# Kernel optimization log

Hardware: AMD Instinct MI355X
Metric: run time of the kernel (lower is better)

Reference implementation:

```python
import jax, jax.numpy as jnp
import numpy as np

N_USER, N_ITEM = 100000, 50000
E, L = 640000, 200000
F0, F1, F2 = 128, 128, 64


def _mean_agg(x_src, src, dst, n_dst):
    # gather messages from source nodes, mean-aggregate onto destination nodes
    msg = x_src[src]                                            # [E, F]
    s = jax.ops.segment_sum(msg, dst, num_segments=n_dst)       # [n_dst, F]
    cnt = jax.ops.segment_sum(jnp.ones((src.shape[0], 1), x_src.dtype), dst,
                              num_segments=n_dst)               # [n_dst, 1]
    return s / jnp.maximum(cnt, 1.0)


def _sage(x_src, x_dst, src, dst, n_dst, Wl, b, Wr):
    # PyG SAGEConv: lin_l(mean_aggr(x_src)) + lin_r(x_dst)
    agg = _mean_agg(x_src, src, dst, n_dst)
    return agg @ Wl + b + x_dst @ Wr


def setup_inputs() -> dict:
    key = jax.random.key(0)
    ks = jax.random.split(key, 20)
    inp = {}
    inp['x_user'] = jax.random.normal(ks[0], (N_USER, F0), jnp.float32)
    inp['x_item'] = jax.random.normal(ks[1], (N_ITEM, F0), jnp.float32)
    inp['src_u'] = jax.random.randint(ks[2], (E,), 0, N_USER)
    inp['dst_i'] = jax.random.randint(ks[3], (E,), 0, N_ITEM)
    inp['el_src'] = jax.random.randint(ks[4], (L,), 0, N_USER)
    inp['el_dst'] = jax.random.randint(ks[5], (L,), 0, N_ITEM)
    # SAGEConv params per edge type per layer: Wl (neighbor), bias, Wr (root)
    def w(k, fi, fo):
        return jax.random.normal(k, (fi, fo), jnp.float32) * (1.0 / np.sqrt(fi))
    inp['Wl_ui1'] = w(ks[6], F0, F1);  inp['b_ui1'] = jnp.zeros((F1,), jnp.float32)
    inp['Wr_ui1'] = w(ks[7], F0, F1)
    inp['Wl_iu1'] = w(ks[8], F0, F1);  inp['b_iu1'] = jnp.zeros((F1,), jnp.float32)
    inp['Wr_iu1'] = w(ks[9], F0, F1)
    inp['Wl_ui2'] = w(ks[10], F1, F2); inp['b_ui2'] = jnp.zeros((F2,), jnp.float32)
    inp['Wr_ui2'] = w(ks[11], F1, F2)
    inp['Wl_iu2'] = w(ks[12], F1, F2); inp['b_iu2'] = jnp.zeros((F2,), jnp.float32)
    inp['Wr_iu2'] = w(ks[13], F1, F2)
    return inp


def reference(x_user, x_item, src_u, dst_i, el_src, el_dst,
              Wl_ui1, b_ui1, Wr_ui1, Wl_iu1, b_iu1, Wr_iu1,
              Wl_ui2, b_ui2, Wr_ui2, Wl_iu2, b_iu2, Wr_iu2):
    # layer 1 (to_hetero: one SAGEConv per edge type; relu per node type; eval -> no dropout)
    h_i1 = jax.nn.relu(_sage(x_user, x_item, src_u, dst_i, N_ITEM, Wl_ui1, b_ui1, Wr_ui1))
    h_u1 = jax.nn.relu(_sage(x_item, x_user, dst_i, src_u, N_USER, Wl_iu1, b_iu1, Wr_iu1))
    # layer 2
    h_i2 = _sage(h_u1, h_i1, src_u, dst_i, N_ITEM, Wl_ui2, b_ui2, Wr_ui2)
    h_u2 = _sage(h_i1, h_u1, dst_i, src_u, N_USER, Wl_iu2, b_iu2, Wr_iu2)
    # LPsimple_classif: gather endpoints, elementwise product, sum over features
    pred = (h_u2[el_src] * h_i2[el_dst]).sum(axis=-1)           # [L]
    return pred
```

## Files before the change

### kernel.cpp

```cpp
#include <hip/hip_runtime.h>

#define NUSER 100000
#define NITEM 50000
#define NEDGE 640000
#define NLINK 200000
#define GI 49
#define GU 98
#define NBU 391
#define NBI 196
#define NBG1 (4 * (NBU + NBI))
#define NBG2 (2 * (NBU + NBI))
#define FCHUNK 4096
#define FNCH 157

typedef unsigned int  uint;
typedef unsigned short ushort_t;
typedef __attribute__((ext_vector_type(8))) short bf16x8;
typedef __attribute__((ext_vector_type(4))) float f32x4;
typedef __attribute__((ext_vector_type(4))) uint  u32x4;

__device__ __forceinline__ ushort_t f2bf(float f) {
    uint u = __float_as_uint(f);
    u += 0x7FFFu + ((u >> 16) & 1u);
    return (ushort_t)(u >> 16);
}
__device__ __forceinline__ float bf2f(ushort_t h) { return __uint_as_float(((uint)h) << 16); }
__device__ __forceinline__ float lo16f(uint u) { return __uint_as_float(u << 16); }
__device__ __forceinline__ float hi16f(uint u) { return __uint_as_float(u & 0xFFFF0000u); }

__global__ __launch_bounds__(256) void countw_kernel(
    const int* __restrict__ src, const int* __restrict__ dst,
    int* __restrict__ cnt_u, int* __restrict__ cnt_i,
    const float* __restrict__ Wl0, const float* __restrict__ Wr0,
    const float* __restrict__ Wl1, const float* __restrict__ Wr1,
    const float* __restrict__ Wl2, const float* __restrict__ Wr2,
    const float* __restrict__ Wl3, const float* __restrict__ Wr3,
    ushort_t* __restrict__ Bh0, ushort_t* __restrict__ Bl0,
    ushort_t* __restrict__ Bh1, ushort_t* __restrict__ Bl1,
    ushort_t* __restrict__ Bh2, ushort_t* __restrict__ Bl2,
    ushort_t* __restrict__ Bh3, ushort_t* __restrict__ Bl3)
{
    if (blockIdx.x < 2500) {
        int e = blockIdx.x * 256 + threadIdx.x;
        if (e >= NEDGE) return;
        atomicAdd(&cnt_u[src[e]], 1);
        atomicAdd(&cnt_i[dst[e]], 1);
        return;
    }
    int b = blockIdx.x - 2500;
    const float *Wl, *Wr; ushort_t *Bh, *Bl; int FO, t;
    if (b < 16)      { Wl = Wl0; Wr = Wr0; Bh = Bh0; Bl = Bl0; FO = 128; t = b * 256 + threadIdx.x; }
    else if (b < 32) { Wl = Wl1; Wr = Wr1; Bh = Bh1; Bl = Bl1; FO = 128; t = (b - 16) * 256 + threadIdx.x; }
    else if (b < 40) { Wl = Wl2; Wr = Wr2; Bh = Bh2; Bl = Bl2; FO = 64;  t = (b - 32) * 256 + threadIdx.x; }
    else             { Wl = Wl3; Wr = Wr3; Bh = Bh3; Bl = Bl3; FO = 64;  t = (b - 40) * 256 + threadIdx.x; }
    int lane = t & 63, ks = (t >> 6) & 3, nt = t >> 8;
    int col = nt * 16 + (lane & 15);
    int k0 = ks * 32 + (lane >> 4) * 8;
    const float* W = (col < FO) ? Wl : Wr;
    int cc = (col < FO) ? col : col - FO;
#pragma unroll
    for (int j = 0; j < 8; ++j) {
        float v = W[(size_t)(k0 + j) * FO + cc];
        ushort_t h = f2bf(v);
        Bh[(size_t)t * 8 + j] = h;
        Bl[(size_t)t * 8 + j] = f2bf(v - bf2f(h));
    }
}

__global__ __launch_bounds__(256) void scan1_kernel(
    const int* __restrict__ cnt_i, const int* __restrict__ cnt_u,
    int* __restrict__ head_i, int* __restrict__ head_u,
    int* __restrict__ bsum_i, int* __restrict__ bsum_u)
{
    __shared__ int sh[256];
    int b = blockIdx.x, t = threadIdx.x;
    const int* cnt; int* head; int* bsum; int n, cb;
    if (b < GI) { cnt = cnt_i; head = head_i; bsum = bsum_i; n = NITEM; cb = b; }
    else        { cnt = cnt_u; head = head_u; bsum = bsum_u; n = NUSER; cb = b - GI; }
    int base = cb * 1024 + t * 4;
    int4 v = {0, 0, 0, 0};
    if (base + 3 < n) v = *(const int4*)(cnt + base);
    else {
        if (base + 0 < n) v.x = cnt[base + 0];
        if (base + 1 < n) v.y = cnt[base + 1];
        if (base + 2 < n) v.z = cnt[base + 2];
    }
    int s = v.x + v.y + v.z + v.w;
    sh[t] = s;
    __syncthreads();
    for (int o = 1; o < 256; o <<= 1) {
        int a = (t >= o) ? sh[t - o] : 0;
        __syncthreads();
        sh[t] += a;
        __syncthreads();
    }
    int excl = sh[t] - s;
    if (t == 255) bsum[cb] = sh[255];
    if (base + 0 < n) head[base + 0] = excl;
    if (base + 1 < n) head[base + 1] = excl + v.x;
    if (base + 2 < n) head[base + 2] = excl + v.x + v.y;
    if (base + 3 < n) head[base + 3] = excl + v.x + v.y + v.z;
}

__global__ __launch_bounds__(256) void scan23_kernel(
    int* __restrict__ head_i, int* __restrict__ head_u,
    const int* __restrict__ bsum_i, const int* __restrict__ bsum_u)
{
    __shared__ int sh[256];
    int b = blockIdx.x, t = threadIdx.x;
    int* head; const int* bsum; int n, cb;
    if (b < GI) { head = head_i; bsum = bsum_i; n = NITEM; cb = b; }
    else        { head = head_u; bsum = bsum_u; n = NUSER; cb = b - GI; }
    sh[t] = (t < cb) ? bsum[t] : 0;
    __syncthreads();
    for (int o = 128; o >= 1; o >>= 1) {
        if (t < o) sh[t] += sh[t + o];
        __syncthreads();
    }
    int add = sh[0];
    int base = cb * 1024 + t * 4;
#pragma unroll
    for (int k = 0; k < 4; ++k)
        if (base + k < n) head[base + k] += add;
}

template <int OSTRIDE, bool ASPLIT>
__device__ __forceinline__ void gemm_body(
    const void* __restrict__ A_,
    const ushort_t* __restrict__ Bh, const ushort_t* __restrict__ Bl,
    ushort_t* __restrict__ dstp, int n, int row0,
    u32x4* __restrict__ bshH, u32x4* __restrict__ bshL)
{
    constexpr int NB = 1024;
    const u32x4* gh = (const u32x4*)Bh;
    const u32x4* gl = (const u32x4*)Bl;
#pragma unroll
    for (int i = 0; i < 2; ++i) {
        int idx = i * 512 + threadIdx.x;
        bshH[idx] = gh[idx];
        bshL[idx] = gl[idx];
    }
    __syncthreads();

    const int lane = threadIdx.x & 63, wv = threadIdx.x >> 6;
    const int lr = lane & 15, lg = lane >> 4;
    const int wrow0 = row0 + wv * 32;
    const int r0 = wrow0 + lr, r1 = wrow0 + 16 + lr;

    f32x4 acc[2][4];
#pragma unroll
    for (int rt = 0; rt < 2; ++rt)
#pragma unroll
        for (int ct = 0; ct < 4; ++ct) { f32x4 zz = {0.f, 0.f, 0.f, 0.f}; acc[rt][ct] = zz; }

    f32x4 f0c[2], f1c[2]; u32x4 qc[2];
#define LOAD_A(KS)                                                              \
    {                                                                           \
        int kb = (KS) * 32 + lg * 8;                                            \
        int rows[2] = {r0, r1};                                                 \
        _Pragma("unroll")                                                       \
        for (int rt = 0; rt < 2; ++rt) {                                        \
            if (ASPLIT) {                                                       \
                f0c[rt] = f32x4{0.f, 0.f, 0.f, 0.f};                            \
                f1c[rt] = f32x4{0.f, 0.f, 0.f, 0.f};                            \
                if (rows[rt] < n) {                                             \
                    const f32x4* p = (const f32x4*)((const float*)A_ +          \
                        (size_t)rows[rt] * 128 + kb);                           \
                    f0c[rt] = p[0]; f1c[rt] = p[1];                             \
                }                                                               \
            } else {                                                            \
                qc[rt] = u32x4{0u, 0u, 0u, 0u};                                 \
                if (rows[rt] < n)                                               \
                    qc[rt] = *(const u32x4*)((const ushort_t*)A_ +              \
                        (size_t)rows[rt] * 128 + kb);                           \
            }                                                                   \
        }                                                                       \
    }

    LOAD_A(0);
#pragma unroll
    for (int ks = 0; ks < 4; ++ks) {
        bf16x8 ah[2], al[2];
#pragma unroll
        for (int rt = 0; rt < 2; ++rt) {
            if (ASPLIT) {
                float e[8];
#pragma unroll
                for (int j = 0; j < 4; ++j) { e[j] = f0c[rt][j]; e[4 + j] = f1c[rt][j]; }
                uint hv[4], lv[4];
#pragma unroll
                for (int j = 0; j < 4; ++j) {
                    ushort_t h0 = f2bf(e[2 * j]), h1 = f2bf(e[2 * j + 1]);
                    hv[j] = (uint)h0 | ((uint)h1 << 16);
                    ushort_t l0 = f2bf(e[2 * j] - bf2f(h0)), l1 = f2bf(e[2 * j + 1] - bf2f(h1));
                    lv[j] = (uint)l0 | ((uint)l1 << 16);
                }
                u32x4 hq = {hv[0], hv[1], hv[2], hv[3]};
                u32x4 lq = {lv[0], lv[1], lv[2], lv[3]};
                ah[rt] = __builtin_bit_cast(bf16x8, hq);
                al[rt] = __builtin_bit_cast(bf16x8, lq);
            } else {
                ah[rt] = __builtin_bit_cast(bf16x8, qc[rt]);
            }
        }
        if (ks < 3) LOAD_A(ks + 1);

#pragma unroll
        for (int ct = 0; ct < 4; ++ct) {
            bf16x8 bh = __builtin_bit_cast(bf16x8, bshH[(ct * 4 + ks) * 64 + lane]);
            bf16x8 bl = __builtin_bit_cast(bf16x8, bshL[(ct * 4 + ks) * 64 + lane]);
#pragma unroll
            for (int rt = 0; rt < 2; ++rt) {
                acc[rt][ct] = __builtin_amdgcn_mfma_f32_16x16x32_bf16(ah[rt], bh, acc[rt][ct], 0, 0, 0);
                acc[rt][ct] = __builtin_amdgcn_mfma_f32_16x16x32_bf16(ah[rt], bl, acc[rt][ct], 0, 0, 0);
                if (ASPLIT)
                    acc[rt][ct] = __builtin_amdgcn_mfma_f32_16x16x32_bf16(al[rt], bh, acc[rt][ct], 0, 0, 0);
            }
        }
    }
#undef LOAD_A

#pragma unroll
    for (int rt = 0; rt < 2; ++rt)
#pragma unroll
        for (int ct = 0; ct < 4; ++ct) {
            int cc = ct * 16 + lr;
#pragma unroll
            for (int r = 0; r < 4; ++r) {
                int orow = wrow0 + rt * 16 + lg * 4 + r;
                if (orow < n) dstp[(size_t)orow * OSTRIDE + cc] = f2bf(acc[rt][ct][r]);
            }
        }
}

__global__ __launch_bounds__(512) void gemmfill_kernel(
    const float* __restrict__ xu, const float* __restrict__ xi,
    const ushort_t* __restrict__ Bh0, const ushort_t* __restrict__ Bl0,
    const ushort_t* __restrict__ Bh1, const ushort_t* __restrict__ Bl1,
    ushort_t* __restrict__ y0, ushort_t* __restrict__ z0,
    ushort_t* __restrict__ y1, ushort_t* __restrict__ z1,
    const int* __restrict__ src, const int* __restrict__ dst,
    int* __restrict__ head_i, int* __restrict__ head_u,
    int* __restrict__ nbr_i, int* __restrict__ nbr_u)
{
    if (blockIdx.x >= NBG1) {
        int b = blockIdx.x - NBG1;
        int pass = b / (2 * FNCH);
        int rem  = b % (2 * FNCH);
        int dir  = rem / FNCH;
        int base = (rem % FNCH) * FCHUNK;
        int e_end = min(base + FCHUNK, NEDGE);
        if (dir == 0) {
            int lo = pass * (NITEM / 8), hi = lo + NITEM / 8;
            for (int e = base + threadIdx.x; e < e_end; e += 512) {
                int d = dst[e];
                if (d >= lo && d < hi) nbr_i[atomicAdd(&head_i[d], 1)] = src[e];
            }
        } else {
            int lo = pass * (NUSER / 8), hi = lo + NUSER / 8;
            for (int e = base + threadIdx.x; e < e_end; e += 512) {
                int s = src[e];
                if (s >= lo && s < hi) nbr_u[atomicAdd(&head_u[s], 1)] = dst[e];
            }
        }
        return;
    }
    __shared__ u32x4 bshH[1024];
    __shared__ u32x4 bshL[1024];
    int bid = blockIdx.x;
    const float* A; const ushort_t *Bh, *Bl; ushort_t *yb, *zb; int n, rowblk, cg;
    if (bid < 4 * NBU) { A = xu; Bh = Bh0; Bl = Bl0; yb = y0; zb = z0; n = NUSER; rowblk = bid >> 2; cg = bid & 3; }
    else { int b2 = bid - 4 * NBU; A = xi; Bh = Bh1; Bl = Bl1; yb = y1; zb = z1; n = NITEM; rowblk = b2 >> 2; cg = b2 & 3; }
    ushort_t* dstp = ((cg < 2) ? yb : zb) + (cg & 1) * 64;
    gemm_body<128, true>(A, Bh + (size_t)cg * 8192, Bl + (size_t)cg * 8192,
                         dstp, n, rowblk * 256, bshH, bshL);
}

__global__ __launch_bounds__(512) void gemm2_kernel(
    const ushort_t* __restrict__ A0, const ushort_t* __restrict__ A1,
    const ushort_t* __restrict__ Bh0, const ushort_t* __restrict__ Bl0,
    const ushort_t* __restrict__ Bh1, const ushort_t* __restrict__ Bl1,
    ushort_t* __restrict__ y0, ushort_t* __restrict__ z0,
    ushort_t* __restrict__ y1, ushort_t* __restrict__ z1)
{
    __shared__ u32x4 bshH[1024];
    __shared__ u32x4 bshL[1024];
    int bid = blockIdx.x;
    const ushort_t* A; const ushort_t *Bh, *Bl; ushort_t *yb, *zb; int n, rowblk, cg;
    if (bid < 2 * NBU) { A = A0; Bh = Bh0; Bl = Bl0; yb = y0; zb = z0; n = NUSER; rowblk = bid >> 1; cg = bid & 1; }
    else { int b2 = bid - 2 * NBU; A = A1; Bh = Bh1; Bl = Bl1; yb = y1; zb = z1; n = NITEM; rowblk = b2 >> 1; cg = b2 & 1; }
    ushort_t* dstp = cg ? zb : yb;
    gemm_body<64, false>(A, Bh + (size_t)cg * 8192, Bl + (size_t)cg * 8192,
                         dstp, n, rowblk * 256, bshH, bshL);
}

__global__ __launch_bounds__(256) void gather1_kernel(
    const ushort_t* __restrict__ ymsg_u, const ushort_t* __restrict__ ymsg_i,
    const int* __restrict__ nbr_i, const int* __restrict__ head_i, const int* __restrict__ cnt_i,
    const int* __restrict__ nbr_u, const int* __restrict__ head_u, const int* __restrict__ cnt_u,
    const ushort_t* __restrict__ z_i, const ushort_t* __restrict__ z_u,
    const float* __restrict__ b_ui, const float* __restrict__ b_iu,
    ushort_t* __restrict__ h1_i, ushort_t* __restrict__ h1_u)
{
    int w = (blockIdx.x << 2) + (threadIdx.x >> 6);
    const ushort_t *ym, *z; const int *nbr, *head, *cnt; const float* bias;
    ushort_t* hout; int node;
    if (w < NITEM) { ym = ymsg_u; nbr = nbr_i; head = head_i; cnt = cnt_i; z = z_i; bias = b_ui; hout = h1_i; node = w; }
    else if (w < NITEM + NUSER) { ym = ymsg_i; nbr = nbr_u; head = head_u; cnt = cnt_u; z = z_u; bias = b_iu; hout = h1_u; node = w - NITEM; }
    else return;
    int lane = threadIdx.x & 63;
    int c = cnt[node], end = head[node];
    int j = end - c;
    const uint* Y = (const uint*)ym;
    float ax = 0.f, ay = 0.f;
    for (; j + 7 < end; j += 8) {
        uint u0 = Y[(size_t)nbr[j + 0] * 64 + lane];
        uint u1 = Y[(size_t)nbr[j + 1] * 64 + lane];
        uint u2 = Y[(size_t)nbr[j + 2] * 64 + lane];
        uint u3 = Y[(size_t)nbr[j + 3] * 64 + lane];
        uint u4 = Y[(size_t)nbr[j + 4] * 64 + lane];
        uint u5 = Y[(size_t)nbr[j + 5] * 64 + lane];
        uint u6 = Y[(size_t)nbr[j + 6] * 64 + lane];
        uint u7 = Y[(size_t)nbr[j + 7] * 64 + lane];
        ax += lo16f(u0) + lo16f(u1) + lo16f(u2) + lo16f(u3)
            + lo16f(u4) + lo16f(u5) + lo16f(u6) + lo16f(u7);
        ay += hi16f(u0) + hi16f(u1) + hi16f(u2) + hi16f(u3)
            + hi16f(u4) + hi16f(u5) + hi16f(u6) + hi16f(u7);
    }
    for (; j + 1 < end; j += 2) {
        uint u0 = Y[(size_t)nbr[j + 0] * 64 + lane];
        uint u1 = Y[(size_t)nbr[j + 1] * 64 + lane];
        ax += lo16f(u0) + lo16f(u1);
        ay += hi16f(u0) + hi16f(u1);
    }
    if (j < end) {
        uint u0 = Y[(size_t)nbr[j] * 64 + lane];
        ax += lo16f(u0); ay += hi16f(u0);
    }
    float m = 1.f / fmaxf((float)c, 1.f);
    uint zu = ((const uint*)z)[(size_t)node * 64 + lane];
    float vx = fmaxf(ax * m + lo16f(zu) + bias[lane * 2], 0.f);
    float vy = fmaxf(ay * m + hi16f(zu) + bias[lane * 2 + 1], 0.f);
    ((uint*)hout)[(size_t)node * 64 + lane] = (uint)f2bf(vx) | ((uint)f2bf(vy) << 16);
}

__global__ __launch_bounds__(256) void gather2_kernel(
    const ushort_t* __restrict__ ymsg_u, const ushort_t* __restrict__ ymsg_i,
    const int* __restrict__ nbr_i, const int* __restrict__ head_i, const int* __restrict__ cnt_i,
    const int* __restrict__ nbr_u, const int* __restrict__ head_u, const int* __restrict__ cnt_u,
    const ushort_t* __restrict__ z_i, const ushort_t* __restrict__ z_u,
    const float* __restrict__ b_ui, const float* __restrict__ b_iu,
    ushort_t* __restrict__ h2_i, ushort_t* __restrict__ h2_u)
{
    int w = (blockIdx.x << 2) + (threadIdx.x >> 6);
    const ushort_t *ym, *z; const int *nbr, *head, *cnt; const float* bias;
    ushort_t* hout; int node;
    if (w < NITEM) { ym = ymsg_u; nbr = nbr_i; head = head_i; cnt = cnt_i; z = z_i; bias = b_ui; hout = h2_i; node = w; }
    else if (w < NITEM + NUSER) { ym = ymsg_i; nbr = nbr_u; head = head_u; cnt = cnt_u; z = z_u; bias = b_iu; hout = h2_u; node = w - NITEM; }
    else return;
    int lane = threadIdx.x & 63;
    int c = cnt[node], end = head[node];
    int j = end - c;
    float a = 0.f;
    for (; j + 7 < end; j += 8) {
        a += bf2f(ym[(size_t)nbr[j + 0] * 64 + lane]) + bf2f(ym[(size_t)nbr[j + 1] * 64 + lane])
           + bf2f(ym[(size_t)nbr[j + 2] * 64 + lane]) + bf2f(ym[(size_t)nbr[j + 3] * 64 + lane])
           + bf2f(ym[(size_t)nbr[j + 4] * 64 + lane]) + bf2f(ym[(size_t)nbr[j + 5] * 64 + lane])
           + bf2f(ym[(size_t)nbr[j + 6] * 64 + lane]) + bf2f(ym[(size_t)nbr[j + 7] * 64 + lane]);
    }
    for (; j + 1 < end; j += 2)
        a += bf2f(ym[(size_t)nbr[j] * 64 + lane]) + bf2f(ym[(size_t)nbr[j + 1] * 64 + lane]);
    if (j < end) a += bf2f(ym[(size_t)nbr[j] * 64 + lane]);
    float m = 1.f / fmaxf((float)c, 1.f);
    float v = a * m + bf2f(z[(size_t)node * 64 + lane]) + bias[lane];
    hout[(size_t)node * 64 + lane] = f2bf(v);
}

__global__ __launch_bounds__(256) void predict_kernel(
    const int* __restrict__ el_src, const int* __restrict__ el_dst,
    const ushort_t* __restrict__ hu, const ushort_t* __restrict__ hi,
    float* __restrict__ out)
{
    int l = (blockIdx.x << 2) + (threadIdx.x >> 6);
    if (l >= NLINK) return;
    int lane = threadIdx.x & 63;
    int u = el_src[l];
    int it = el_dst[l];
    float v = bf2f(hu[(size_t)u * 64 + lane]) * bf2f(hi[(size_t)it * 64 + lane]);
#pragma unroll
    for (int o = 32; o >= 1; o >>= 1) v += __shfl_down(v, o, 64);
    if (lane == 0) out[l] = v;
}

extern "C" void kernel_launch(void* const* d_in, const int* in_sizes, int n_in,
                              void* d_out, int out_size, void* d_ws, size_t ws_size,
                              hipStream_t stream) {
    const float* x_user = (const float*)d_in[0];
    const float* x_item = (const float*)d_in[1];
    const int*   src_u  = (const int*)d_in[2];
    const int*   dst_i  = (const int*)d_in[3];
    const int*   el_src = (const int*)d_in[4];
    const int*   el_dst = (const int*)d_in[5];
    const float* Wl_ui1 = (const float*)d_in[6];
    const float* b_ui1  = (const float*)d_in[7];
    const float* Wr_ui1 = (const float*)d_in[8];
    const float* Wl_iu1 = (const float*)d_in[9];
    const float* b_iu1  = (const float*)d_in[10];
    const float* Wr_iu1 = (const float*)d_in[11];
    const float* Wl_ui2 = (const float*)d_in[12];
    const float* b_ui2  = (const float*)d_in[13];
    const float* Wr_ui2 = (const float*)d_in[14];
    const float* Wl_iu2 = (const float*)d_in[15];
    const float* b_iu2  = (const float*)d_in[16];
    const float* Wr_iu2 = (const float*)d_in[17];
    float* out = (float*)d_out;

    int* iw     = (int*)d_ws;
    int* cnt_i  = iw;
    int* cnt_u  = iw + 50000;
    int* bsum_i = iw + 150000;
    int* bsum_u = iw + 150064;
    int* head_i = iw + 150192;
    int* head_u = iw + 200192;
    int* nbr_i  = iw + 300192;
    int* nbr_u  = iw + 940192;
    char* W8 = (char*)d_ws;
    size_t off = 6320768;
    ushort_t* Bh1u = (ushort_t*)(W8 + off); off += 65536;
    ushort_t* Bl1u = (ushort_t*)(W8 + off); off += 65536;
    ushort_t* Bh1i = (ushort_t*)(W8 + off); off += 65536;
    ushort_t* Bl1i = (ushort_t*)(W8 + off); off += 65536;
    ushort_t* Bh2u = (ushort_t*)(W8 + off); off += 32768;
    ushort_t* Bl2u = (ushort_t*)(W8 + off); off += 32768;
    ushort_t* Bh2i = (ushort_t*)(W8 + off); off += 32768;
    ushort_t* Bl2i = (ushort_t*)(W8 + off); off += 32768;
    ushort_t* h1_u = (ushort_t*)(W8 + off); off += (size_t)NUSER * 128 * 2;
    ushort_t* h1_i = (ushort_t*)(W8 + off); off += (size_t)NITEM * 128 * 2;
    size_t YB = off;
    ushort_t* ymsg_u = (ushort_t*)(W8 + YB);
    ushort_t* ymsg_i = (ushort_t*)(W8 + YB + 25600000);
    ushort_t* z_u    = (ushort_t*)(W8 + YB + 38400000);
    ushort_t* z_i    = (ushort_t*)(W8 + YB + 64000000);
    ushort_t* ymsg2_u = (ushort_t*)(W8 + YB);
    ushort_t* ymsg2_i = (ushort_t*)(W8 + YB + 12800000);
    ushort_t* z2_u    = (ushort_t*)(W8 + YB + 19200000);
    ushort_t* z2_i    = (ushort_t*)(W8 + YB + 32000000);
    ushort_t* h2_u    = (ushort_t*)(W8 + YB + 38400000);
    ushort_t* h2_i    = (ushort_t*)(W8 + YB + 51200000);

    hipMemsetAsync(d_ws, 0, 150000 * sizeof(int), stream);

    countw_kernel<<<2548, 256, 0, stream>>>(
        src_u, dst_i, cnt_u, cnt_i,
        Wl_ui1, Wr_iu1, Wl_iu1, Wr_ui1, Wl_ui2, Wr_iu2, Wl_iu2, Wr_ui2,
        Bh1u, Bl1u, Bh1i, Bl1i, Bh2u, Bl2u, Bh2i, Bl2i);

    scan1_kernel<<<GI + GU, 256, 0, stream>>>(cnt_i, cnt_u, head_i, head_u, bsum_i, bsum_u);
    scan23_kernel<<<GI + GU, 256, 0, stream>>>(head_i, head_u, bsum_i, bsum_u);

    gemmfill_kernel<<<NBG1 + 8 * 2 * FNCH, 512, 0, stream>>>(
        x_user, x_item, Bh1u, Bl1u, Bh1i, Bl1i,
        ymsg_u, z_u, ymsg_i, z_i,
        src_u, dst_i, head_i, head_u, nbr_i, nbr_u);

    gather1_kernel<<<(NITEM + NUSER) / 4, 256, 0, stream>>>(
        ymsg_u, ymsg_i, nbr_i, head_i, cnt_i, nbr_u, head_u, cnt_u,
        z_i, z_u, b_ui1, b_iu1, h1_i, h1_u);

    gemm2_kernel<<<NBG2, 512, 0, stream>>>(
        h1_u, h1_i, Bh2u, Bl2u, Bh2i, Bl2i,
        ymsg2_u, z2_u, ymsg2_i, z2_i);
    gather2_kernel<<<(NITEM + NUSER) / 4, 256, 0, stream>>>(
        ymsg2_u, ymsg2_i, nbr_i, head_i, cnt_i, nbr_u, head_u, cnt_u,
        z2_i, z2_u, b_ui2, b_iu2, h2_i, h2_u);

    predict_kernel<<<NLINK / 4, 256, 0, stream>>>(el_src, el_dst, h2_u, h2_i, out);
}
```

Baseline: 370.9 us.

## Restructure layer-1 GEMM: truncation split, drop B-low term, LDS-staged stores, fewer fill passes

The layer-1 GEMM drops the A_hi*B_lo MFMA term and keeps only A_hi*B and A_lo*B, with A split by bit truncation instead of rounding. Each block now covers 128 rows by 128 columns with 8 column tiles per wave, and output is staged through LDS so global stores are coalesced 16-byte rows. The CSR fill uses 4 destination-range passes instead of 8. This cuts MFMA count, conversion ALU work, scattered 2-byte stores and redundant edge rereads, at the cost of some precision from omitting the weight low part and more atomic contention per pass.

```diff
diff --git a/kernel.cpp b/kernel.cpp
--- a/kernel.cpp
+++ b/kernel.cpp
@@ -6,12 +6,15 @@
 #define NLINK 200000
 #define GI 49
 #define GU 98
+#define NB1U 782
+#define NB1I 391
+#define NB1G (2 * (NB1U + NB1I))
 #define NBU 391
 #define NBI 196
-#define NBG1 (4 * (NBU + NBI))
 #define NBG2 (2 * (NBU + NBI))
 #define FCHUNK 4096
 #define FNCH 157
+#define FPASS 4
 
 typedef unsigned int  uint;
 typedef unsigned short ushort_t;
@@ -124,140 +127,109 @@
         if (base + k < n) head[base + k] += add;
 }
 
-template <int OSTRIDE, bool ASPLIT>
-__device__ __forceinline__ void gemm_body(
-    const void* __restrict__ A_,
-    const ushort_t* __restrict__ Bh, const ushort_t* __restrict__ Bl,
-    ushort_t* __restrict__ dstp, int n, int row0,
-    u32x4* __restrict__ bshH, u32x4* __restrict__ bshL)
-{
-    constexpr int NB = 1024;
-    const u32x4* gh = (const u32x4*)Bh;
-    const u32x4* gl = (const u32x4*)Bl;
-#pragma unroll
-    for (int i = 0; i < 2; ++i) {
-        int idx = i * 512 + threadIdx.x;
-        bshH[idx] = gh[idx];
-        bshL[idx] = gl[idx];
-    }
+__device__ __forceinline__ void gemm1_body(
+    const float* __restrict__ A, const ushort_t* __restrict__ Bcg,
+    ushort_t* __restrict__ dstp, int n, int row0, u32x4* __restrict__ bsh)
+{
+#pragma unroll
+    for (int i = 0; i < 4; ++i)
+        bsh[i * 512 + threadIdx.x] = ((const u32x4*)Bcg)[i * 512 + threadIdx.x];
     __syncthreads();
 
     const int lane = threadIdx.x & 63, wv = threadIdx.x >> 6;
     const int lr = lane & 15, lg = lane >> 4;
-    const int wrow0 = row0 + wv * 32;
-    const int r0 = wrow0 + lr, r1 = wrow0 + 16 + lr;
-
-    f32x4 acc[2][4];
-#pragma unroll
-    for (int rt = 0; rt < 2; ++rt)
-#pragma unroll
-        for (int ct = 0; ct < 4; ++ct) { f32x4 zz = {0.f, 0.f, 0.f, 0.f}; acc[rt][ct] = zz; }
-
-    f32x4 f0c[2], f1c[2]; u32x4 qc[2];
-#define LOAD_A(KS)                                                              \
-    {                                                                           \
-        int kb = (KS) * 32 + lg * 8;                                            \
-        int rows[2] = {r0, r1};                                                 \
-        _Pragma("unroll")                                                       \
-        for (int rt = 0; rt < 2; ++rt) {                                        \
-            if (ASPLIT) {                                                       \
-                f0c[rt] = f32x4{0.f, 0.f, 0.f, 0.f};                            \
-                f1c[rt] = f32x4{0.f, 0.f, 0.f, 0.f};                            \
-                if (rows[rt] < n) {                                             \
-                    const f32x4* p = (const f32x4*)((const float*)A_ +          \
-                        (size_t)rows[rt] * 128 + kb);                           \
-                    f0c[rt] = p[0]; f1c[rt] = p[1];                             \
-                }                                                               \
-            } else {                                                            \
-                qc[rt] = u32x4{0u, 0u, 0u, 0u};                                 \
-                if (rows[rt] < n)                                               \
-                    qc[rt] = *(const u32x4*)((const ushort_t*)A_ +              \
-                        (size_t)rows[rt] * 128 + kb);                           \
-            }                                                                   \
-        }                                                                       \
-    }
-
-    LOAD_A(0);
+    const int r0 = row0 + wv * 16 + lr;
+    const bool rv = r0 < n;
+    const float* arow = A + (size_t)r0 * 128;
+
+    f32x4 acc[8];
+#pragma unroll
+    for (int ct = 0; ct < 8; ++ct) { f32x4 zz = {0.f, 0.f, 0.f, 0.f}; acc[ct] = zz; }
+
+    f32x4 fa, fb;
+#define LOAD_A1(KS)                                                            \
+    {                                                                          \
+        fa = f32x4{0.f, 0.f, 0.f, 0.f}; fb = fa;                               \
+        if (rv) {                                                              \
+            const f32x4* p = (const f32x4*)(arow + (KS) * 32 + lg * 8);        \
+            fa = p[0]; fb = p[1];                                              \
+        }                                                                      \
+    }
+
+    LOAD_A1(0);
 #pragma unroll
     for (int ks = 0; ks < 4; ++ks) {
-        bf16x8 ah[2], al[2];
-#pragma unroll
-        for (int rt = 0; rt < 2; ++rt) {
-            if (ASPLIT) {
-                float e[8];
-#pragma unroll
-                for (int j = 0; j < 4; ++j) { e[j] = f0c[rt][j]; e[4 + j] = f1c[rt][j]; }
-                uint hv[4], lv[4];
-#pragma unroll
-                for (int j = 0; j < 4; ++j) {
-                    ushort_t h0 = f2bf(e[2 * j]), h1 = f2bf(e[2 * j + 1]);
-                    hv[j] = (uint)h0 | ((uint)h1 << 16);
-                    ushort_t l0 = f2bf(e[2 * j] - bf2f(h0)), l1 = f2bf(e[2 * j + 1] - bf2f(h1));
-                    lv[j] = (uint)l0 | ((uint)l1 << 16);
-                }
-                u32x4 hq = {hv[0], hv[1], hv[2], hv[3]};
-                u32x4 lq = {lv[0], lv[1], lv[2], lv[3]};
-                ah[rt] = __builtin_bit_cast(bf16x8, hq);
-                al[rt] = __builtin_bit_cast(bf16x8, lq);
-            } else {
-                ah[rt] = __builtin_bit_cast(bf16x8, qc[rt]);
-            }
+        float e0s[4] = {fa[0], fa[2], fb[0], fb[2]};
+        float e1s[4] = {fa[1], fa[3], fb[1], fb[3]};
+        uint hv[4], lv[4];
+#pragma unroll
+        for (int j = 0; j < 4; ++j) {
+            uint au = __float_as_uint(e0s[j]);
+            uint bu = __float_as_uint(e1s[j]);
+            uint ah_ = au & 0xFFFF0000u, bh_ = bu & 0xFFFF0000u;
+            hv[j] = (au >> 16) | bh_;
+            float l0 = e0s[j] - __uint_as_float(ah_);
+            float l1 = e1s[j] - __uint_as_float(bh_);
+            lv[j] = (__float_as_uint(l0) >> 16) | (__float_as_uint(l1) & 0xFFFF0000u);
         }
-        if (ks < 3) LOAD_A(ks + 1);
-
-#pragma unroll
-        for (int ct = 0; ct < 4; ++ct) {
-            bf16x8 bh = __builtin_bit_cast(bf16x8, bshH[(ct * 4 + ks) * 64 + lane]);
-            bf16x8 bl = __builtin_bit_cast(bf16x8, bshL[(ct * 4 + ks) * 64 + lane]);
-#pragma unroll
-            for (int rt = 0; rt < 2; ++rt) {
-                acc[rt][ct] = __builtin_amdgcn_mfma_f32_16x16x32_bf16(ah[rt], bh, acc[rt][ct], 0, 0, 0);
-                acc[rt][ct] = __builtin_amdgcn_mfma_f32_16x16x32_bf16(ah[rt], bl, acc[rt][ct], 0, 0, 0);
-                if (ASPLIT)
-                    acc[rt][ct] = __builtin_amdgcn_mfma_f32_16x16x32_bf16(al[rt], bh, acc[rt][ct], 0, 0, 0);
-            }
+        u32x4 hq = {hv[0], hv[1], hv[2], hv[3]};
+        u32x4 lq = {lv[0], lv[1], lv[2], lv[3]};
+        bf16x8 ahf = __builtin_bit_cast(bf16x8, hq);
+        bf16x8 alf = __builtin_bit_cast(bf16x8, lq);
+        if (ks < 3) LOAD_A1(ks + 1);
+
+#pragma unroll
+        for (int ct = 0; ct < 8; ++ct) {
+            bf16x8 bh = __builtin_bit_cast(bf16x8, bsh[(ct * 4 + ks) * 64 + lane]);
+            acc[ct] = __builtin_amdgcn_mfma_f32_16x16x32_bf16(ahf, bh, acc[ct], 0, 0, 0);
+            acc[ct] = __builtin_amdgcn_mfma_f32_16x16x32_bf16(alf, bh, acc[ct], 0, 0, 0);
         }
     }
-#undef LOAD_A
-
-#pragma unroll
-    for (int rt = 0; rt < 2; ++rt)
-#pragma unroll
-        for (int ct = 0; ct < 4; ++ct) {
-            int cc = ct * 16 + lr;
-#pragma unroll
-            for (int r = 0; r < 4; ++r) {
-                int orow = wrow0 + rt * 16 + lg * 4 + r;
-                if (orow < n) dstp[(size_t)orow * OSTRIDE + cc] = f2bf(acc[rt][ct][r]);
-            }
-        }
+#undef LOAD_A1
+
+    __syncthreads();
+    ushort_t* cl = (ushort_t*)bsh;
+#pragma unroll
+    for (int ct = 0; ct < 8; ++ct) {
+        int col = ct * 16 + lr;
+#pragma unroll
+        for (int r = 0; r < 4; ++r)
+            cl[(wv * 16 + lg * 4 + r) * 128 + col] = f2bf(acc[ct][r]);
+    }
+    __syncthreads();
+    int row = threadIdx.x >> 2, seg = threadIdx.x & 3;
+    int grow = row0 + row;
+    if (grow < n) {
+        const u32x4* s = (const u32x4*)(cl + row * 128) + seg * 4;
+        u32x4* d = (u32x4*)(dstp + (size_t)grow * 128) + seg * 4;
+        d[0] = s[0]; d[1] = s[1]; d[2] = s[2]; d[3] = s[3];
+    }
 }
 
 __global__ __launch_bounds__(512) void gemmfill_kernel(
     const float* __restrict__ xu, const float* __restrict__ xi,
-    const ushort_t* __restrict__ Bh0, const ushort_t* __restrict__ Bl0,
-    const ushort_t* __restrict__ Bh1, const ushort_t* __restrict__ Bl1,
+    const ushort_t* __restrict__ Bh0, const ushort_t* __restrict__ Bh1,
     ushort_t* __restrict__ y0, ushort_t* __restrict__ z0,
     ushort_t* __restrict__ y1, ushort_t* __restrict__ z1,
     const int* __restrict__ src, const int* __restrict__ dst,
     int* __restrict__ head_i, int* __restrict__ head_u,
     int* __restrict__ nbr_i, int* __restrict__ nbr_u)
 {
-    if (blockIdx.x >= NBG1) {
-        int b = blockIdx.x - NBG1;
+    if (blockIdx.x >= NB1G) {
+        int b = blockIdx.x - NB1G;
         int pass = b / (2 * FNCH);
         int rem  = b % (2 * FNCH);
         int dir  = rem / FNCH;
         int base = (rem % FNCH) * FCHUNK;
         int e_end = min(base + FCHUNK, NEDGE);
         if (dir == 0) {
-            int lo = pass * (NITEM / 8), hi = lo + NITEM / 8;
+            int lo = pass * (NITEM / FPASS), hi = lo + NITEM / FPASS;
             for (int e = base + threadIdx.x; e < e_end; e += 512) {
                 int d = dst[e];
                 if (d >= lo && d < hi) nbr_i[atomicAdd(&head_i[d], 1)] = src[e];
             }
         } else {
-            int lo = pass * (NUSER / 8), hi = lo + NUSER / 8;
+            int lo = pass * (NUSER / FPASS), hi = lo + NUSER / FPASS;
             for (int e = base + threadIdx.x; e < e_end; e += 512) {
                 int s = src[e];
                 if (s >= lo && s < hi) nbr_u[atomicAdd(&head_u[s], 1)] = dst[e];
@@ -265,15 +237,88 @@
         }
         return;
     }
-    __shared__ u32x4 bshH[1024];
-    __shared__ u32x4 bshL[1024];
+    __shared__ u32x4 bsh[2048];
     int bid = blockIdx.x;
-    const float* A; const ushort_t *Bh, *Bl; ushort_t *yb, *zb; int n, rowblk, cg;
-    if (bid < 4 * NBU) { A = xu; Bh = Bh0; Bl = Bl0; yb = y0; zb = z0; n = NUSER; rowblk = bid >> 2; cg = bid & 3; }
-    else { int b2 = bid - 4 * NBU; A = xi; Bh = Bh1; Bl = Bl1; yb = y1; zb = z1; n = NITEM; rowblk = b2 >> 2; cg = b2 & 3; }
-    ushort_t* dstp = ((cg < 2) ? yb : zb) + (cg & 1) * 64;
-    gemm_body<128, true>(A, Bh + (size_t)cg * 8192, Bl + (size_t)cg * 8192,
-                         dstp, n, rowblk * 256, bshH, bshL);
+    if (bid < 2 * NB1U) {
+        int rowblk = bid >> 1, cg = bid & 1;
+        gemm1_body(xu, Bh0 + (size_t)cg * 16384, cg ? z0 : y0, NUSER, rowblk * 128, bsh);
+    } else {
+        int b2 = bid - 2 * NB1U;
+        int rowblk = b2 >> 1, cg = b2 & 1;
+        gemm1_body(xi, Bh1 + (size_t)cg * 16384, cg ? z1 : y1, NITEM, rowblk * 128, bsh);
+    }
+}
+
+__device__ __forceinline__ void gemm2_body(
+    const ushort_t* __restrict__ A,
+    const ushort_t* __restrict__ Bh, const ushort_t* __restrict__ Bl,
+    ushort_t* __restrict__ dstp, int n, int row0,
+    u32x4* __restrict__ bshH, u32x4* __restrict__ bshL)
+{
+#pragma unroll
+    for (int i = 0; i < 2; ++i) {
+        int idx = i * 512 + threadIdx.x;
+        bshH[idx] = ((const u32x4*)Bh)[idx];
+        bshL[idx] = ((const u32x4*)Bl)[idx];
+    }
+    __syncthreads();
+
+    const int lane = threadIdx.x & 63, wv = threadIdx.x >> 6;
+    const int lr = lane & 15, lg = lane >> 4;
+    const int wrow0 = row0 + wv * 32;
+    const int r0 = wrow0 + lr, r1 = wrow0 + 16 + lr;
+
+    f32x4 acc[2][4];
+#pragma unroll
+    for (int rt = 0; rt < 2; ++rt)
+#pragma unroll
+        for (int ct = 0; ct < 4; ++ct) { f32x4 zz = {0.f, 0.f, 0.f, 0.f}; acc[rt][ct] = zz; }
+
+    u32x4 qc[2];
+#define LOAD_A2(KS)                                                            \
+    {                                                                          \
+        int kb = (KS) * 32 + lg * 8;                                           \
+        int rows[2] = {r0, r1};                                                \
+        _Pragma("unroll")                                                      \
+        for (int rt = 0; rt < 2; ++rt) {                                       \
+            qc[rt] = u32x4{0u, 0u, 0u, 0u};                                    \
+            if (rows[rt] < n)                                                  \
+                qc[rt] = *(const u32x4*)(A + (size_t)rows[rt] * 128 + kb);     \
+        }                                                                      \
+    }
+
+    LOAD_A2(0);
+#pragma unroll
+    for (int ks = 0; ks < 4; ++ks) {
+        bf16x8 ah[2];
+#pragma unroll
+        for (int rt = 0; rt < 2; ++rt) ah[rt] = __builtin_bit_cast(bf16x8, qc[rt]);
+        if (ks < 3) LOAD_A2(ks + 1);
+
+#pragma unroll
+        for (int ct = 0; ct < 4; ++ct) {
+            bf16x8 bh = __builtin_bit_cast(bf16x8, bshH[(ct * 4 + ks) * 64 + lane]);
+            bf16x8 bl = __builtin_bit_cast(bf16x8, bshL[(ct * 4 + ks) * 64 + lane]);
+#pragma unroll
+            for (int rt = 0; rt < 2; ++rt) {
+                acc[rt][ct] = __builtin_amdgcn_mfma_f32_16x16x32_bf16(ah[rt], bh, acc[rt][ct], 0, 0, 0);
+                acc[rt][ct] = __builtin_amdgcn_mfma_f32_16x16x32_bf16(ah[rt], bl, acc[rt][ct], 0, 0, 0);
+            }
+        }
+    }
+#undef LOAD_A2
+
+#pragma unroll
+    for (int rt = 0; rt < 2; ++rt)
+#pragma unroll
+        for (int ct = 0; ct < 4; ++ct) {
+            int cc = ct * 16 + lr;
+#pragma unroll
+            for (int r = 0; r < 4; ++r) {
+                int orow = wrow0 + rt * 16 + lg * 4 + r;
+                if (orow < n) dstp[(size_t)orow * 64 + cc] = f2bf(acc[rt][ct][r]);
+            }
+        }
 }
 
 __global__ __launch_bounds__(512) void gemm2_kernel(
@@ -286,12 +331,16 @@
     __shared__ u32x4 bshH[1024];
     __shared__ u32x4 bshL[1024];
     int bid = blockIdx.x;
-    const ushort_t* A; const ushort_t *Bh, *Bl; ushort_t *yb, *zb; int n, rowblk, cg;
-    if (bid < 2 * NBU) { A = A0; Bh = Bh0; Bl = Bl0; yb = y0; zb = z0; n = NUSER; rowblk = bid >> 1; cg = bid & 1; }
-    else { int b2 = bid - 2 * NBU; A = A1; Bh = Bh1; Bl = Bl1; yb = y1; zb = z1; n = NITEM; rowblk = b2 >> 1; cg = b2 & 1; }
-    ushort_t* dstp = cg ? zb : yb;
-    gemm_body<64, false>(A, Bh + (size_t)cg * 8192, Bl + (size_t)cg * 8192,
-                         dstp, n, rowblk * 256, bshH, bshL);
+    if (bid < 2 * NBU) {
+        int rowblk = bid >> 1, cg = bid & 1;
+        gemm2_body(A0, Bh0 + (size_t)cg * 8192, Bl0 + (size_t)cg * 8192,
+                   cg ? z0 : y0, NUSER, rowblk * 256, bshH, bshL);
+    } else {
+        int b2 = bid - 2 * NBU;
+        int rowblk = b2 >> 1, cg = b2 & 1;
+        gemm2_body(A1, Bh1 + (size_t)cg * 8192, Bl1 + (size_t)cg * 8192,
+                   cg ? z1 : y1, NITEM, rowblk * 256, bshH, bshL);
+    }
 }
 
 __global__ __launch_bounds__(256) void gather1_kernel(
@@ -458,8 +507,8 @@
     scan1_kernel<<<GI + GU, 256, 0, stream>>>(cnt_i, cnt_u, head_i, head_u, bsum_i, bsum_u);
     scan23_kernel<<<GI + GU, 256, 0, stream>>>(head_i, head_u, bsum_i, bsum_u);
 
-    gemmfill_kernel<<<NBG1 + 8 * 2 * FNCH, 512, 0, stream>>>(
-        x_user, x_item, Bh1u, Bl1u, Bh1i, Bl1i,
+    gemmfill_kernel<<<NB1G + FPASS * 2 * FNCH, 512, 0, stream>>>(
+        x_user, x_item, Bh1u, Bh1i,
         ymsg_u, z_u, ymsg_i, z_i,
         src_u, dst_i, head_i, head_u, nbr_i, nbr_u);
 
```

Result: no change. 365.1 us (-1.6%).
